# Kernel tuning notes

Measured on AMD Instinct MI355X. Metric: run time of the kernel, lower is better.

The kernel has to match this reference:

```python
import jax, jax.numpy as jnp
import numpy as np

B, T, C, H = 4, 4096, 2048, 128


def setup_inputs() -> dict:
    key = jax.random.key(0)
    ks = jax.random.split(key, 7)
    s = 0.02
    return {
        "x": jax.random.normal(ks[0], (B, T, C), dtype=jnp.float32),
        "Wk": jax.random.normal(ks[1], (C, H), dtype=jnp.float32) * s,
        "bk": jax.random.normal(ks[2], (H,), dtype=jnp.float32) * s,
        "Wq": jax.random.normal(ks[3], (C, H), dtype=jnp.float32) * s,
        "bq": jax.random.normal(ks[4], (H,), dtype=jnp.float32) * s,
        "Wv": jax.random.normal(ks[5], (C, H), dtype=jnp.float32) * s,
        "bv": jax.random.normal(ks[6], (H,), dtype=jnp.float32) * s,
    }


def reference(x, Wk, bk, Wq, bq, Wv, bv):
    # x: [B, T, C]
    Bq, Tq, Cq = x.shape
    k = x @ Wk + bk  # [B, T, H]
    q = x @ Wq + bq
    v = x @ Wv + bv
    # NOTE: original scales by C**-0.5 (input emb dim), faithfully reproduced.
    scale = jnp.asarray(Cq, x.dtype) ** -0.5
    wei = jnp.einsum("bth,bsh->bts", q, k) * scale  # [B, T, T]
    causal = jnp.tril(jnp.ones((Tq, Tq), dtype=bool))
    wei = jnp.where(causal, wei, -jnp.inf)
    wei = jax.nn.softmax(wei, axis=-1)
    # dropout omitted (inference/eval mode)
    return jnp.einsum("bts,bsh->bth", wei, v)  # [B, T, H]
```

## Files before the change

kernel.cpp:

```cpp
#include <hip/hip_runtime.h>
#include <hip/hip_bf16.h>
#include <stdint.h>

#define T_SEQ 4096
#define C_DIM 2048
#define H_DIM 128
#define NBATCH 4

typedef unsigned short u16;
typedef __attribute__((ext_vector_type(8))) __bf16 bf16x8;
typedef __attribute__((ext_vector_type(4))) float f32x4;
typedef __attribute__((ext_vector_type(8))) unsigned short u16x8;
typedef __attribute__((ext_vector_type(4))) unsigned short u16x4;

__device__ __forceinline__ u16 f2bf(float f) {
  union { float f; uint32_t i; } v; v.f = f;
  uint32_t r = v.i + 0x7FFFu + ((v.i >> 16) & 1u);
  return (u16)(r >> 16);
}
__device__ __forceinline__ float bf2f(u16 u) {
  union { uint32_t i; float f; } v; v.i = ((uint32_t)u) << 16;
  return v.f;
}

__device__ __forceinline__ void gload16(const void* g, void* l) {
  __builtin_amdgcn_global_load_lds(
      (__attribute__((address_space(1))) void*)(g),
      (__attribute__((address_space(3))) void*)(l), 16, 0, 0);
}

__device__ __forceinline__ f32x4 mfma_bf16(bf16x8 a, bf16x8 b, f32x4 c) {
  return __builtin_amdgcn_mfma_f32_16x16x32_bf16(a, b, c, 0, 0, 0);
}

template<int CTRL>
__device__ __forceinline__ float dpp_mov(float x) {
  return __int_as_float(__builtin_amdgcn_mov_dpp(__float_as_int(x), CTRL, 0xF, 0xF, true));
}
__device__ __forceinline__ float red16_max(float v) {
  v = fmaxf(v, dpp_mov<0x121>(v));
  v = fmaxf(v, dpp_mov<0x122>(v));
  v = fmaxf(v, dpp_mov<0x124>(v));
  v = fmaxf(v, dpp_mov<0x128>(v));
  return v;
}
__device__ __forceinline__ float red16_sum(float v) {
  v += dpp_mov<0x121>(v);
  v += dpp_mov<0x122>(v);
  v += dpp_mov<0x124>(v);
  v += dpp_mov<0x128>(v);
  return v;
}

__global__ __launch_bounds__(256) void transpose_w(
    const float* __restrict__ Wq, const float* __restrict__ Wk,
    const float* __restrict__ Wv, u16* __restrict__ Wt)
{
  __shared__ u16 Wl[64 * 72];
  const int bk = blockIdx.x;
  const int bn = blockIdx.y;
  const int p  = blockIdx.z;
  const float* W = (p == 0) ? Wq : (p == 1) ? Wk : Wv;
  const int t = threadIdx.x;

  for (int ps = 0; ps < 16; ++ps) {
    int e  = ps * 256 + t;
    int kk = e >> 6, nn = e & 63;
    Wl[kk * 72 + nn] = f2bf(W[(size_t)(bk * 64 + kk) * H_DIM + bn * 64 + nn]);
  }
  __syncthreads();
  for (int ps = 0; ps < 16; ++ps) {
    int o  = ps * 256 + t;
    int nl = o >> 6, kl = o & 63;
    int n  = bn * 64 + nl;
    int g  = kl >> 3, j = kl & 7;
    int ks = ((g ^ (n & 7)) << 3) | j;
    Wt[(size_t)p * (H_DIM * C_DIM) + (size_t)n * C_DIM + bk * 64 + kl] = Wl[ks * 72 + nl];
  }
}

__global__ __launch_bounds__(512, 1) void qkv_fused(
    const float* __restrict__ x, const u16* __restrict__ Wt,
    const float* __restrict__ bq, const float* __restrict__ bk, const float* __restrict__ bv,
    u16* __restrict__ qo, u16* __restrict__ ko, u16* __restrict__ vTo)
{
  __shared__ alignas(16) u16 SMEM[2][28672];

  const int tid  = threadIdx.x;
  const int w    = tid >> 6, lane = tid & 63;
  const int t16  = lane & 15, quad = lane >> 4;
  const int mh   = w >> 2;
  const int nq   = w & 3;
  const int rt   = blockIdx.x;

  f32x4 acc[2][6];
  for (int i = 0; i < 2; ++i)
    for (int j = 0; j < 6; ++j) acc[i][j] = f32x4{0.f, 0.f, 0.f, 0.f};

  const size_t rowBase = (size_t)rt * 64;
  const int arow = tid >> 3;
  const int ag   = tid & 7;
  const float* xrow = &x[(rowBase + arow) * C_DIM + ag * 8];

  float4 a0 = ((const float4*)(xrow))[0];
  float4 a1 = ((const float4*)(xrow))[1];
  {
    u16* As = SMEM[0];
    u16* Bs = SMEM[0] + 4096;
    for (int p = 0; p < 3; ++p) {
      const u16* Wp = Wt + (size_t)p * (H_DIM * C_DIM);
      for (int j = 0; j < 2; ++j) {
        int e8 = (((j << 3) + w) * 64 + lane) * 8;
        int rr = e8 >> 6, kk = e8 & 63;
        gload16(Wp + (size_t)rr * C_DIM + kk, &Bs[p * 8192 + e8]);
      }
    }
    u16x8 pk;
    pk[0] = f2bf(a0.x); pk[1] = f2bf(a0.y); pk[2] = f2bf(a0.z); pk[3] = f2bf(a0.w);
    pk[4] = f2bf(a1.x); pk[5] = f2bf(a1.y); pk[6] = f2bf(a1.z); pk[7] = f2bf(a1.w);
    *(u16x8*)&As[arow * 64 + ((ag ^ (arow & 7)) << 3)] = pk;
  }
  a0 = ((const float4*)(xrow + 64))[0];
  a1 = ((const float4*)(xrow + 64))[1];

  for (int it = 0; it < 32; ++it) {
    const int cur = it & 1, nxt = cur ^ 1;
    __syncthreads();

    if (it + 1 < 32) {
      const int k1 = (it + 1) * 64;
      u16* As = SMEM[nxt];
      u16* Bs = SMEM[nxt] + 4096;
      for (int p = 0; p < 3; ++p) {
        const u16* Wp = Wt + (size_t)p * (H_DIM * C_DIM);
        for (int j = 0; j < 2; ++j) {
          int e8 = (((j << 3) + w) * 64 + lane) * 8;
          int rr = e8 >> 6, kk = e8 & 63;
          gload16(Wp + (size_t)rr * C_DIM + k1 + kk, &Bs[p * 8192 + e8]);
        }
      }
      u16x8 pk;
      pk[0] = f2bf(a0.x); pk[1] = f2bf(a0.y); pk[2] = f2bf(a0.z); pk[3] = f2bf(a0.w);
      pk[4] = f2bf(a1.x); pk[5] = f2bf(a1.y); pk[6] = f2bf(a1.z); pk[7] = f2bf(a1.w);
      *(u16x8*)&As[arow * 64 + ((ag ^ (arow & 7)) << 3)] = pk;
      if (it + 2 < 32) {
        const float4* xp = (const float4*)(xrow + (it + 2) * 64);
        a0 = xp[0]; a1 = xp[1];
      }
    }

    u16* As = SMEM[cur];
    u16* Bs = SMEM[cur] + 4096;
    for (int ks = 0; ks < 2; ++ks) {
      bf16x8 af[2], bfr[6];
      for (int ra = 0; ra < 2; ++ra)
        af[ra] = *(const bf16x8*)&As[(mh * 32 + ra * 16 + t16) * 64 +
                                     (((ks * 4 + quad) ^ (t16 & 7)) << 3)];
      for (int c = 0; c < 6; ++c) {
        int col = nq * 96 + c * 16 + t16;
        int p = col >> 7, pc = col & 127;
        bfr[c] = *(const bf16x8*)&Bs[p * 8192 + pc * 64 +
                                     (((ks * 4 + quad) ^ (t16 & 7)) << 3)];
      }
      for (int ra = 0; ra < 2; ++ra)
        for (int c = 0; c < 6; ++c)
          acc[ra][c] = mfma_bf16(af[ra], bfr[c], acc[ra][c]);
    }
  }

  __syncthreads();
  u16* Oq = SMEM[0];
  u16* Ok = SMEM[0] + 8192;
  u16* Ov = SMEM[0] + 16384;

  const float QSCALE = 0.022097086912079612f;
  for (int c = 0; c < 6; ++c) {
    int col = nq * 96 + c * 16 + t16;
    int p = col >> 7, pc = col & 127;
    float bias = (p == 0) ? bq[pc] : (p == 1) ? bk[pc] : bv[pc];
    for (int ra = 0; ra < 2; ++ra) {
      for (int r = 0; r < 4; ++r) {
        int row16 = mh * 32 + ra * 16 + quad * 4 + r;
        float v = acc[ra][c][r] + bias;
        if (p == 0) v *= QSCALE;
        if (p == 2) {
          int gt = row16 >> 3;
          Ov[pc * 64 + ((gt ^ (pc & 7)) << 3) + (row16 & 7)] = f2bf(v);
        } else {
          u16* O = (p == 0) ? Oq : Ok;
          int g = pc >> 3;
          O[row16 * 128 + (((g ^ (row16 & 15)) << 3) | (pc & 7))] = f2bf(v);
        }
      }
    }
  }
  __syncthreads();

  const int bb = rt >> 6;
  const int tb = (rt & 63) * 64;
  for (int ps = 0; ps < 2; ++ps) {
    int c = ps * 512 + tid;
    {
      int row16 = c >> 4, g = c & 15;
      u16x8 v = *(const u16x8*)&Oq[row16 * 128 + ((g ^ (row16 & 15)) << 3)];
      *(u16x8*)&qo[(rowBase + row16) * H_DIM + g * 8] = v;
    }
    *(u16x8*)&ko[rowBase * H_DIM + c * 8] = *(const u16x8*)&Ok[c * 8];
    {
      int d = c >> 3, gc = c & 7;
      *(u16x8*)&vTo[((size_t)bb * H_DIM + d) * T_SEQ + tb + gc * 8] =
          *(const u16x8*)&Ov[c * 8];
    }
  }
}

__global__ __launch_bounds__(256, 2) void flash_attn(
    const u16* __restrict__ q, const u16* __restrict__ k,
    const u16* __restrict__ vT, float* __restrict__ out,
    void* __restrict__ OpartRaw, float* __restrict__ MLpart,
    int split, int pf32)
{
  __shared__ alignas(16) u16 Kt[2][64 * 128];
  __shared__ alignas(16) u16 Vt[2][128 * 64];
  __shared__ alignas(16) u16 Ps[4 * 16 * 72];

  const int tid  = threadIdx.x;
  const int w    = tid >> 6, lane = tid & 63;
  const int t16  = lane & 15, quad = lane >> 4;
  const int b    = blockIdx.x;

  int qt, kt0, ktn, mls, esd;
  if (split) {
    const int j = blockIdx.y;
    int c, n;
    if (j < 64)       { qt = 63 - (j >> 2); c = j & 3; n = 4; }
    else if (j < 112) { int t = j - 64; int d3 = t / 3; qt = 47 - d3; c = t - d3 * 3; n = 3; }
    else if (j < 144) { int t = j - 112; qt = 31 - (t >> 1); c = t & 1; n = 2; }
    else              { qt = 159 - j; c = 0; n = 1; }
    const int NT = qt + 1;
    kt0 = c * NT / n;
    ktn = (c + 1) * NT / n - kt0;
    if (n == 1) { mls = -1; esd = -1; }
    else {
      int mlb, esb;
      if (qt >= 48)      { mlb = (qt - 48) * 4;       esb = (qt - 48) * 3; }
      else if (qt >= 32) { mlb = 64 + (qt - 32) * 3;  esb = 48 + (qt - 32) * 2; }
      else               { mlb = 112 + (qt - 16) * 2; esb = 80 + (qt - 16); }
      mls = b * 144 + mlb + c;
      esd = (c >= 1) ? (b * 96 + esb + c - 1) : -2;
    }
  } else {
    qt = 63 - blockIdx.y; kt0 = 0; ktn = qt + 1; mls = -1; esd = -1;
  }

  const float L2E = 1.4426950408889634f;

  bf16x8 qf[4];
  {
    const u16* qrow = q + ((size_t)(b * T_SEQ + qt * 64 + w * 16 + t16)) * H_DIM;
    for (int c = 0; c < 4; ++c)
      qf[c] = *(const bf16x8*)(qrow + c * 32 + quad * 8);
  }

  f32x4 Oc[8];
  for (int i = 0; i < 8; ++i) Oc[i] = f32x4{0.f, 0.f, 0.f, 0.f};
  float mrow[4] = {-1e30f, -1e30f, -1e30f, -1e30f};
  float lrow[4] = {0.f, 0.f, 0.f, 0.f};

  const u16* kbase = k  + ((size_t)b * T_SEQ) * H_DIM;
  const u16* vbase = vT + ((size_t)b * H_DIM) * T_SEQ;

  {
    const u16* kg = kbase + (size_t)(kt0 * 64) * H_DIM;
    for (int j = 0; j < 4; ++j) {
      int e8 = (((j << 2) + w) * 64 + lane) * 8;
      gload16(kg + e8, &Kt[0][e8]);
      int d = e8 >> 6, kk = e8 & 63;
      gload16(vbase + (size_t)d * T_SEQ + kt0 * 64 + kk, &Vt[0][e8]);
    }
  }

  int cur = 0;
  for (int it = 0; it < ktn; ++it) {
    const int kt = kt0 + it;
    __syncthreads();
    if (it + 1 < ktn) {
      const int nb = cur ^ 1, kt1 = kt + 1;
      const u16* kg = kbase + (size_t)(kt1 * 64) * H_DIM;
      for (int j = 0; j < 4; ++j) {
        int e8 = (((j << 2) + w) * 64 + lane) * 8;
        gload16(kg + e8, &Kt[nb][e8]);
        int d = e8 >> 6, kk = e8 & 63;
        gload16(vbase + (size_t)d * T_SEQ + kt1 * 64 + kk, &Vt[nb][e8]);
      }
    }

    f32x4 S[4];
    for (int ct = 0; ct < 4; ++ct) S[ct] = f32x4{0.f, 0.f, 0.f, 0.f};
    __builtin_amdgcn_s_setprio(1);
    for (int c = 0; c < 4; ++c) {
      for (int ct = 0; ct < 4; ++ct) {
        bf16x8 kf = *(const bf16x8*)&Kt[cur][(ct * 16 + t16) * H_DIM +
                                            (((c * 4 + quad) ^ t16) << 3)];
        S[ct] = mfma_bf16(qf[c], kf, S[ct]);
      }
    }
    __builtin_amdgcn_s_setprio(0);

    if (kt == qt) {
      for (int ct = 0; ct < 4; ++ct)
        for (int r = 0; r < 4; ++r)
          if (ct * 16 + t16 > w * 16 + quad * 4 + r) S[ct][r] = -1e30f;
    }

    float alpha[4];
    bool any = false;
    for (int r = 0; r < 4; ++r) {
      float mx = red16_max(fmaxf(fmaxf(S[0][r], S[1][r]), fmaxf(S[2][r], S[3][r])));
      if (mx > mrow[r] + 8.0f) {
        alpha[r] = exp2f((mrow[r] - mx) * L2E);
        mrow[r] = mx;
        any = true;
      } else {
        alpha[r] = 1.0f;
      }
    }
    if (any) {
      for (int r = 0; r < 4; ++r) lrow[r] *= alpha[r];
      for (int dt = 0; dt < 8; ++dt)
        for (int r = 0; r < 4; ++r)
          Oc[dt][r] *= alpha[r];
    }
    for (int r = 0; r < 4; ++r) {
      float s = 0.f;
      for (int ct = 0; ct < 4; ++ct) {
        float pv = exp2f((S[ct][r] - mrow[r]) * L2E);
        S[ct][r] = pv;
        s += pv;
      }
      lrow[r] += red16_sum(s);
    }

    u16* pw = &Ps[w * 1152];
    for (int ct = 0; ct < 4; ++ct)
      for (int r = 0; r < 4; ++r)
        pw[(quad * 4 + r) * 72 + ct * 16 + t16] = f2bf(S[ct][r]);
    __asm__ volatile("s_waitcnt lgkmcnt(0)" ::: "memory");

    __builtin_amdgcn_s_setprio(1);
    for (int ks = 0; ks < 2; ++ks) {
      bf16x8 pf = *(const bf16x8*)&pw[t16 * 72 + ks * 32 + quad * 8];
      for (int dt = 0; dt < 8; ++dt) {
        bf16x8 vf = *(const bf16x8*)&Vt[cur][(dt * 16 + t16) * 64 +
                                            (((ks * 4 + quad) ^ (t16 & 7)) << 3)];
        Oc[dt] = mfma_bf16(pf, vf, Oc[dt]);
      }
    }
    __builtin_amdgcn_s_setprio(0);
    cur ^= 1;
  }

  if (mls < 0) {
    for (int r = 0; r < 4; ++r) {
      float inv = 1.0f / lrow[r];
      size_t row = (size_t)b * T_SEQ + qt * 64 + w * 16 + quad * 4 + r;
      for (int dt = 0; dt < 8; ++dt)
        out[row * H_DIM + dt * 16 + t16] = Oc[dt][r] * inv;
    }
  } else {
    if (t16 == 0)
      for (int r = 0; r < 4; ++r) {
        int row = w * 16 + quad * 4 + r;
        MLpart[(size_t)mls * 128 + row * 2 + 0] = mrow[r];
        MLpart[(size_t)mls * 128 + row * 2 + 1] = lrow[r];
      }
    if (esd == -2) {
      for (int r = 0; r < 4; ++r) {
        size_t row = (size_t)b * T_SEQ + qt * 64 + w * 16 + quad * 4 + r;
        for (int dt = 0; dt < 8; ++dt)
          out[row * H_DIM + dt * 16 + t16] = Oc[dt][r];
      }
    } else if (pf32) {
      float* op = (float*)OpartRaw + (size_t)esd * 8192;
      for (int r = 0; r < 4; ++r) {
        int row = w * 16 + quad * 4 + r;
        for (int dt = 0; dt < 8; ++dt)
          op[row * 128 + dt * 16 + t16] = Oc[dt][r];
      }
    } else {
      u16* op = (u16*)OpartRaw + (size_t)esd * 8192;
      for (int r = 0; r < 4; ++r) {
        int row = w * 16 + quad * 4 + r;
        for (int dt = 0; dt < 8; ++dt)
          op[row * 128 + dt * 16 + t16] = f2bf(Oc[dt][r]);
      }
    }
  }
}

__global__ __launch_bounds__(256) void combine(
    const void* __restrict__ OpartRaw, const float* __restrict__ MLpart,
    float* __restrict__ out, int pf32)
{
  __shared__ float cs[4][64];
  const float L2E = 1.4426950408889634f;
  const int s = blockIdx.x;
  const int b = s / 48, qt = 16 + (s % 48);
  const int t = threadIdx.x;

  int n, mlb, esb;
  if (qt >= 48)      { n = 4; mlb = (qt - 48) * 4;       esb = (qt - 48) * 3; }
  else if (qt >= 32) { n = 3; mlb = 64 + (qt - 32) * 3;  esb = 48 + (qt - 32) * 2; }
  else               { n = 2; mlb = 112 + (qt - 16) * 2; esb = 80 + (qt - 16); }
  const int mls0 = b * 144 + mlb;
  const int esd0 = b * 96 + esb;

  if (t < 64) {
    float m[4], l[4];
    float mg = -1e30f;
    for (int c = 0; c < n; ++c) {
      const float* ML = MLpart + (size_t)(mls0 + c) * 128;
      m[c] = ML[t * 2]; l[c] = ML[t * 2 + 1];
      mg = fmaxf(mg, m[c]);
    }
    float denom = 0.f, e[4];
    for (int c = 0; c < n; ++c) {
      e[c] = exp2f((m[c] - mg) * L2E);
      denom += l[c] * e[c];
    }
    float inv = 1.0f / denom;
    for (int c = 0; c < n; ++c) cs[c][t] = e[c] * inv;
  }
  __syncthreads();

  float* o = out + ((size_t)b * T_SEQ + (size_t)qt * 64) * (size_t)H_DIM;
  for (int i4 = t; i4 < 2048; i4 += 256) {
    const int row = i4 >> 5;
    float4 acc = ((float4*)o)[i4];
    const float c0 = cs[0][row];
    acc.x *= c0; acc.y *= c0; acc.z *= c0; acc.w *= c0;
    for (int c = 1; c < n; ++c) {
      const float cc = cs[c][row];
      if (pf32) {
        const float4 p = ((const float4*)((const float*)OpartRaw +
                          (size_t)(esd0 + c - 1) * 8192))[i4];
        acc.x += p.x * cc; acc.y += p.y * cc;
        acc.z += p.z * cc; acc.w += p.w * cc;
      } else {
        const u16x4 p = ((const u16x4*)((const u16*)OpartRaw +
                         (size_t)(esd0 + c - 1) * 8192))[i4];
        acc.x += bf2f(p[0]) * cc; acc.y += bf2f(p[1]) * cc;
        acc.z += bf2f(p[2]) * cc; acc.w += bf2f(p[3]) * cc;
      }
    }
    ((float4*)o)[i4] = acc;
  }
}

extern "C" void kernel_launch(void* const* d_in, const int* in_sizes, int n_in,
                              void* d_out, int out_size, void* d_ws, size_t ws_size,
                              hipStream_t stream) {
  const float* x  = (const float*)d_in[0];
  const float* Wk = (const float*)d_in[1];
  const float* bk = (const float*)d_in[2];
  const float* Wq = (const float*)d_in[3];
  const float* bq = (const float*)d_in[4];
  const float* Wv = (const float*)d_in[5];
  const float* bv = (const float*)d_in[6];
  float* out = (float*)d_out;

  char* ws = (char*)d_ws;
  u16* qb  = (u16*)(ws);
  u16* kb  = (u16*)(ws + 4194304);
  u16* vT  = (u16*)(ws + 8388608);
  u16* Wt  = (u16*)(ws + 12582912);
  void* Opart = (void*)(ws + 14155776);

  const size_t base     = 14155776ull;
  const size_t ml_bytes = 294912ull;
  const size_t need_f32 = base + 12582912ull + ml_bytes;
  const size_t need_b16 = base + 6291456ull  + ml_bytes;

  int split, pf32;
  float* MLpart;
  if (ws_size >= need_f32) {
    split = 1; pf32 = 1;
    MLpart = (float*)(ws + base + 12582912ull);
  } else if (ws_size >= need_b16) {
    split = 1; pf32 = 0;
    MLpart = (float*)(ws + base + 6291456ull);
  } else {
    split = 0; pf32 = 0;
    MLpart = (float*)(ws + base);
  }

  hipLaunchKernelGGL(transpose_w, dim3(32, 2, 3), dim3(256), 0, stream, Wq, Wk, Wv, Wt);
  hipLaunchKernelGGL(qkv_fused, dim3(256), dim3(512), 0, stream,
                     x, Wt, bq, bk, bv, qb, kb, vT);
  hipLaunchKernelGGL(flash_attn, dim3(4, split ? 160 : 64), dim3(256), 0, stream,
                     qb, kb, vT, out, Opart, MLpart, split, pf32);
  if (split)
    hipLaunchKernelGGL(combine, dim3(192), dim3(256), 0, stream, Opart, MLpart, out, pf32);
}
```

Before: 295.8 us.

## Read K and V fragments directly from global memory instead of LDS staging

Removes the double-buffered LDS tiles for K and V along with their async prefetch and per-iteration barrier. MFMA operands are now loaded straight from global memory through the cache, and the occupancy hint rises to three blocks per CU. This cuts LDS usage and synchronisation, but each wave re-fetches K/V from global/L2 with no overlap of the next tile's loads. It keeps the XOR-swizzled offsets, which only index correctly if the stored global layout is already swizzled.

Result: slower. 313.5 us (+6.0%).

```diff
diff --git a/kernel.cpp b/kernel.cpp
--- a/kernel.cpp
+++ b/kernel.cpp
@@ -214,14 +214,12 @@
   }
 }
 
-__global__ __launch_bounds__(256, 2) void flash_attn(
+__global__ __launch_bounds__(256, 3) void flash_attn(
     const u16* __restrict__ q, const u16* __restrict__ k,
     const u16* __restrict__ vT, float* __restrict__ out,
     void* __restrict__ OpartRaw, float* __restrict__ MLpart,
     int split, int pf32)
 {
-  __shared__ alignas(16) u16 Kt[2][64 * 128];
-  __shared__ alignas(16) u16 Vt[2][128 * 64];
   __shared__ alignas(16) u16 Ps[4 * 16 * 72];
 
   const int tid  = threadIdx.x;
@@ -270,38 +268,18 @@
   const u16* kbase = k  + ((size_t)b * T_SEQ) * H_DIM;
   const u16* vbase = vT + ((size_t)b * H_DIM) * T_SEQ;
 
-  {
-    const u16* kg = kbase + (size_t)(kt0 * 64) * H_DIM;
-    for (int j = 0; j < 4; ++j) {
-      int e8 = (((j << 2) + w) * 64 + lane) * 8;
-      gload16(kg + e8, &Kt[0][e8]);
-      int d = e8 >> 6, kk = e8 & 63;
-      gload16(vbase + (size_t)d * T_SEQ + kt0 * 64 + kk, &Vt[0][e8]);
-    }
-  }
-
-  int cur = 0;
   for (int it = 0; it < ktn; ++it) {
     const int kt = kt0 + it;
-    __syncthreads();
-    if (it + 1 < ktn) {
-      const int nb = cur ^ 1, kt1 = kt + 1;
-      const u16* kg = kbase + (size_t)(kt1 * 64) * H_DIM;
-      for (int j = 0; j < 4; ++j) {
-        int e8 = (((j << 2) + w) * 64 + lane) * 8;
-        gload16(kg + e8, &Kt[nb][e8]);
-        int d = e8 >> 6, kk = e8 & 63;
-        gload16(vbase + (size_t)d * T_SEQ + kt1 * 64 + kk, &Vt[nb][e8]);
-      }
-    }
+    const u16* kg = kbase + (size_t)(kt * 64) * H_DIM;
+    const u16* vg = vbase + kt * 64;
 
     f32x4 S[4];
     for (int ct = 0; ct < 4; ++ct) S[ct] = f32x4{0.f, 0.f, 0.f, 0.f};
     __builtin_amdgcn_s_setprio(1);
     for (int c = 0; c < 4; ++c) {
       for (int ct = 0; ct < 4; ++ct) {
-        bf16x8 kf = *(const bf16x8*)&Kt[cur][(ct * 16 + t16) * H_DIM +
-                                            (((c * 4 + quad) ^ t16) << 3)];
+        bf16x8 kf = *(const bf16x8*)&kg[(ct * 16 + t16) * H_DIM +
+                                        (((c * 4 + quad) ^ t16) << 3)];
         S[ct] = mfma_bf16(qf[c], kf, S[ct]);
       }
     }
@@ -351,13 +329,12 @@
     for (int ks = 0; ks < 2; ++ks) {
       bf16x8 pf = *(const bf16x8*)&pw[t16 * 72 + ks * 32 + quad * 8];
       for (int dt = 0; dt < 8; ++dt) {
-        bf16x8 vf = *(const bf16x8*)&Vt[cur][(dt * 16 + t16) * 64 +
-                                            (((ks * 4 + quad) ^ (t16 & 7)) << 3)];
+        bf16x8 vf = *(const bf16x8*)&vg[(size_t)(dt * 16 + t16) * T_SEQ +
+                                        (((ks * 4 + quad) ^ (t16 & 7)) << 3)];
         Oc[dt] = mfma_bf16(pf, vf, Oc[dt]);
       }
     }
     __builtin_amdgcn_s_setprio(0);
-    cur ^= 1;
   }
 
   if (mls < 0) {
```
